# Kernel tuning notes

Hardware: AMD Instinct MI355X
Metric: run time of the kernel (lower is better)

## Reference

```python
import jax, jax.numpy as jnp
import numpy as np

N_NODES = 50000
N_EDGES = 1_600_000
N_DIMS = 64
INTERACT = ((0,), (1,), (0, 1))  # interact index tuples over [hidden_vi, hidden_vj]


def setup_inputs() -> dict:
    key = jax.random.key(0)
    k1, k2, k3 = jax.random.split(key, 3)
    hidden = jax.random.normal(k1, (1, N_NODES, N_DIMS), dtype=jnp.float32)
    pos_weight = jax.random.uniform(k2, (len(INTERACT), N_DIMS), dtype=jnp.float32)
    neg_weight = jax.random.uniform(k3, (len(INTERACT), N_DIMS), dtype=jnp.float32)
    rng = np.random.default_rng(0)
    vi = np.sort(rng.integers(0, N_NODES, size=N_EDGES)).astype(np.int32)  # sorted by vi
    vj = rng.integers(0, N_NODES, size=N_EDGES).astype(np.int32)
    rel = rng.integers(0, 500, size=N_EDGES).astype(np.int32)
    idx = np.zeros(N_EDGES, dtype=np.int32)  # batch_size == 1
    # (idx, vi, vj, rel, idx_vi, idx_vj, new_idx_e2vi, new_idx_e2vj)
    selected_edges = np.stack([idx, vi, vj, rel, vi, vj, vi, vj], axis=1)
    return {
        "hidden": hidden,
        "pos_weight": pos_weight,
        "neg_weight": neg_weight,
        "selected_edges": jnp.asarray(selected_edges),
    }


def _scorer(inputs, pos_weight, neg_weight):
    # inputs: list of [E, D]; returns per-edge scalar logits [E]
    pos_xs, neg_xs = [], []
    for idxs in INTERACT:
        pos_x = jnp.ones((), jnp.float32)
        neg_x = jnp.ones((), jnp.float32)
        for i in idxs:
            pos_x = pos_x * jnp.maximum(inputs[i], 0)
            neg_x = neg_x * (-jnp.minimum(inputs[i], 0))
        pos_xs.append(pos_x)
        neg_xs.append(neg_x)
    pos_xs = jnp.stack(pos_xs, axis=-2)  # [E, n_prod, D]
    neg_xs = jnp.stack(neg_xs, axis=-2)
    logits = jnp.sum(pos_xs * pos_weight, axis=(-2, -1)) - jnp.sum(neg_xs * neg_weight, axis=(-2, -1))
    return logits  # [E]


def reference(hidden, pos_weight, neg_weight, selected_edges):
    n_nodes = hidden.shape[1]
    vi = selected_edges[:, 1]
    vj = selected_edges[:, 2]
    h = hidden[0]  # [N, D], batch_size == 1

    # node2edge gather
    hidden_vi = h[vi]  # [E, D]
    hidden_vj = h[vj]  # [E, D]

    # per-edge attention logits (Scorer)
    logits = _scorer([hidden_vi, hidden_vj], pos_weight, neg_weight)  # [E]

    # neighbor softmax over outgoing edges of vi (sparse segment softmax)
    seg_max = jax.ops.segment_max(logits, vi, num_segments=n_nodes)
    ex = jnp.exp(logits - seg_max[vi])
    denom = jax.ops.segment_sum(ex, vi, num_segments=n_nodes)
    attn = ex / denom[vi]  # [E]

    # aggregate attended messages at vj and scatter back to node tensor
    msg = attn[:, None] * hidden_vi  # [E, D]
    out = jax.ops.segment_sum(msg, vj, num_segments=n_nodes)  # [N, D]
    return out[None]  # [1, N, D]
```

## Files before the change

kernel.cpp:

```cpp
#include <hip/hip_runtime.h>
#include <math.h>

#define NDIM 64

__device__ __forceinline__ unsigned bf16rne(unsigned u) {
    return (u + 0x7fffu + ((u >> 16) & 1u)) >> 16;
}

__global__ void __launch_bounds__(256)
k_prep_pack(const float* __restrict__ h,
            const float* __restrict__ pw, const float* __restrict__ nw,
            unsigned short* __restrict__ h16, float2* __restrict__ s12,
            const int* __restrict__ edges, unsigned* __restrict__ pvivj,
            int* __restrict__ hist,
            int n_nodes, int n_edges, int node_blocks) {
    if ((int)blockIdx.x < node_blocks) {
        const int lane = threadIdx.x & 63;
        const int n = blockIdx.x * 4 + (threadIdx.x >> 6);
        if (n >= n_nodes) return;
        const float a = h[(size_t)n * NDIM + lane];
        const float pa = fmaxf(a, 0.f), na = pa - a;
        float t1 = pa * pw[lane]      - na * nw[lane];
        float t2 = pa * pw[64 + lane] - na * nw[64 + lane];
        #pragma unroll
        for (int m = 32; m >= 1; m >>= 1) {
            t1 += __shfl_xor(t1, m, 64);
            t2 += __shfl_xor(t2, m, 64);
        }
        h16[(size_t)n * NDIM + lane] = (unsigned short)bf16rne(__float_as_uint(a));
        if (lane == 0) s12[n] = make_float2(t1, t2);
    } else {
        const int e = ((int)blockIdx.x - node_blocks) * 256 + threadIdx.x;
        if (e >= n_edges) return;
        const int vi = __builtin_nontemporal_load(edges + (size_t)e * 8 + 1);
        const int vj = __builtin_nontemporal_load(edges + (size_t)e * 8 + 2);
        __builtin_nontemporal_store((unsigned)vi | ((unsigned)vj << 16), pvivj + e);
        atomicAdd(&hist[vj], 1);
    }
}

__global__ void __launch_bounds__(256)
scan_blocks(int* __restrict__ data, int* __restrict__ bsum, int n) {
    __shared__ int sm[256];
    const int t = threadIdx.x;
    const int i = blockIdx.x * 256 + t;
    int v = (i < n) ? data[i] : 0;
    sm[t] = v;
    __syncthreads();
    int x = v;
    #pragma unroll
    for (int off = 1; off < 256; off <<= 1) {
        int add = (t >= off) ? sm[t - off] : 0;
        __syncthreads();
        x += add; sm[t] = x;
        __syncthreads();
    }
    if (i < n) data[i] = x - v;
    if (t == 255) bsum[blockIdx.x] = x;
}

__global__ void __launch_bounds__(256)
scan_top(int* __restrict__ bsum, int nb) {
    __shared__ int sm[256];
    const int t = threadIdx.x;
    const int chunk = (nb + 255) / 256;
    const int beg = t * chunk, end = min(beg + chunk, nb);
    int s = 0;
    for (int i = beg; i < end; ++i) s += bsum[i];
    sm[t] = s;
    __syncthreads();
    int x = s;
    #pragma unroll
    for (int off = 1; off < 256; off <<= 1) {
        int add = (t >= off) ? sm[t - off] : 0;
        __syncthreads();
        x += add; sm[t] = x;
        __syncthreads();
    }
    int run = x - s;
    for (int i = beg; i < end; ++i) { const int v = bsum[i]; bsum[i] = run; run += v; }
}

__global__ void __launch_bounds__(256)
scan_add(int* __restrict__ data, const int* __restrict__ bsum, int n, int total) {
    const int i = blockIdx.x * 256 + threadIdx.x;
    if (i < n) data[i] += bsum[blockIdx.x];
    else if (i == n) data[i] = total;
}

__global__ void __launch_bounds__(256)
k1_fused2(const unsigned* __restrict__ pvivj,
          const unsigned short* __restrict__ h16,
          const float2* __restrict__ s12,
          const float* __restrict__ w2p, const float* __restrict__ w2n,
          float* __restrict__ ex,
          int* __restrict__ offs,
          unsigned* __restrict__ rec,
          int n_edges) {
    const int t = blockIdx.x * 256 + threadIdx.x;
    const int e0 = t * 2;
    if (e0 >= n_edges) return;
    const bool has1 = (e0 + 1 < n_edges);

    const unsigned v0 = pvivj[e0];
    const unsigned v1 = has1 ? pvivj[e0 + 1] : v0;
    const int vi0 = (int)(v0 & 0xffffu), vj0 = (int)(v0 >> 16);
    const int vi1 = (int)(v1 & 0xffffu), vj1 = (int)(v1 >> 16);

    const uint4* hj0 = (const uint4*)(h16 + (size_t)vj0 * NDIM);
    const uint4* hj1 = (const uint4*)(h16 + (size_t)vj1 * NDIM);
    const uint4* hi0 = (const uint4*)(h16 + (size_t)vi0 * NDIM);
    const uint4* hi1 = (const uint4*)(h16 + (size_t)vi1 * NDIM);

    uint4 B0[8], B1[8];
    #pragma unroll
    for (int q = 0; q < 8; ++q) { B0[q] = hj0[q]; B1[q] = hj1[q]; }

    float cp0 = 0.f, cn0 = 0.f, cp1 = 0.f, cn1 = 0.f;
    #pragma unroll
    for (int q = 0; q < 8; ++q) {
        const uint4 ua0 = hi0[q];
        const uint4 ua1 = hi1[q];
        const unsigned a0u[4] = {ua0.x, ua0.y, ua0.z, ua0.w};
        const unsigned a1u[4] = {ua1.x, ua1.y, ua1.z, ua1.w};
        const unsigned b0u[4] = {B0[q].x, B0[q].y, B0[q].z, B0[q].w};
        const unsigned b1u[4] = {B1[q].x, B1[q].y, B1[q].z, B1[q].w};
        #pragma unroll
        for (int k = 0; k < 4; ++k) {
            const int d = q * 8 + k * 2;
            const float w2pd = w2p[d], w2pd1 = w2p[d + 1];
            const float w2nd = w2n[d], w2nd1 = w2n[d + 1];
            {
                const float a0 = __uint_as_float(a0u[k] << 16);
                const float a1 = __uint_as_float(a0u[k] & 0xffff0000u);
                const float b0 = __uint_as_float(b0u[k] << 16);
                const float b1 = __uint_as_float(b0u[k] & 0xffff0000u);
                const float pa0 = fmaxf(a0, 0.f), na0 = pa0 - a0;
                const float pb0 = fmaxf(b0, 0.f), nb0 = pb0 - b0;
                const float pa1 = fmaxf(a1, 0.f), na1 = pa1 - a1;
                const float pb1 = fmaxf(b1, 0.f), nb1 = pb1 - b1;
                cp0 = fmaf(pa0 * pb0, w2pd,  cp0);
                cn0 = fmaf(na0 * nb0, w2nd,  cn0);
                cp0 = fmaf(pa1 * pb1, w2pd1, cp0);
                cn0 = fmaf(na1 * nb1, w2nd1, cn0);
            }
            {
                const float a0 = __uint_as_float(a1u[k] << 16);
                const float a1 = __uint_as_float(a1u[k] & 0xffff0000u);
                const float b0 = __uint_as_float(b1u[k] << 16);
                const float b1 = __uint_as_float(b1u[k] & 0xffff0000u);
                const float pa0 = fmaxf(a0, 0.f), na0 = pa0 - a0;
                const float pb0 = fmaxf(b0, 0.f), nb0 = pb0 - b0;
                const float pa1 = fmaxf(a1, 0.f), na1 = pa1 - a1;
                const float pb1 = fmaxf(b1, 0.f), nb1 = pb1 - b1;
                cp1 = fmaf(pa0 * pb0, w2pd,  cp1);
                cn1 = fmaf(na0 * nb0, w2nd,  cn1);
                cp1 = fmaf(pa1 * pb1, w2pd1, cp1);
                cn1 = fmaf(na1 * nb1, w2nd1, cn1);
            }
        }
    }
    const float2 si0 = s12[vi0], sj0 = s12[vj0];
    const float2 si1 = s12[vi1], sj1 = s12[vj1];
    const float exf0 = __expf(si0.x + sj0.y + cp0 - cn0);
    const float exf1 = __expf(si1.x + sj1.y + cp1 - cn1);

    __builtin_nontemporal_store(exf0, ex + e0);
    const int pos0 = atomicAdd(&offs[vj0], 1);
    rec[pos0] = ((unsigned)vi0 << 16) | bf16rne(__float_as_uint(exf0));
    if (has1) {
        __builtin_nontemporal_store(exf1, ex + e0 + 1);
        const int pos1 = atomicAdd(&offs[vj1], 1);
        rec[pos1] = ((unsigned)vi1 << 16) | bf16rne(__float_as_uint(exf1));
    }
}

__global__ void __launch_bounds__(256)
k2_seg(const unsigned* __restrict__ pvivj, const float* __restrict__ ex,
       float* __restrict__ denom, int n_edges) {
    const int e = blockIdx.x * 256 + threadIdx.x;
    const int lane = threadIdx.x & 63;
    const bool valid = (e < n_edges);
    const int vi = valid ? (int)(pvivj[e] & 0xffffu) : -1;
    float s = valid ? ex[e] : 0.f;
    #pragma unroll
    for (int o = 1; o < 64; o <<= 1) {
        const float pv = __shfl_up(s, o, 64);
        const int   pi = __shfl_up(vi, o, 64);
        if (lane >= o && pi == vi) s += pv;
    }
    const int nvi = __shfl_down(vi, 1, 64);
    if ((lane == 63 || nvi != vi) && vi >= 0)
        atomicAdd(&denom[vi], s);
}

__global__ void __launch_bounds__(256)
k_gmul(const unsigned short* __restrict__ h16, const float* __restrict__ denom,
       unsigned short* __restrict__ g16, int n_nodes) {
    const int lane = threadIdx.x & 63;
    const int n = blockIdx.x * 4 + (threadIdx.x >> 6);
    if (n >= n_nodes) return;
    const float d = denom[n];
    const float r = (d > 0.f) ? 1.f / d : 0.f;
    const float hv = __uint_as_float((unsigned)h16[(size_t)n * NDIM + lane] << 16);
    g16[(size_t)n * NDIM + lane] = (unsigned short)bf16rne(__float_as_uint(hv * r));
}

__global__ void __launch_bounds__(256)
k3b_gather(const unsigned* __restrict__ rec, const int* __restrict__ offs,
           const unsigned short* __restrict__ g16,
           float* __restrict__ out, int n_nodes) {
    const int lane = threadIdx.x & 63;
    const int n = blockIdx.x * 4 + (threadIdx.x >> 6);
    if (n >= n_nodes) return;
    const int beg = (n == 0) ? 0 : offs[n - 1];
    const int end = offs[n];
    float acc = 0.f;
    int k = beg;
    for (; k + 8 <= end; k += 8) {
        unsigned r[8];
        #pragma unroll
        for (int u = 0; u < 8; ++u) r[u] = __builtin_nontemporal_load(rec + k + u);
        float v[8];
        #pragma unroll
        for (int u = 0; u < 8; ++u)
            v[u] = __uint_as_float((unsigned)g16[(size_t)(r[u] >> 16) * NDIM + lane] << 16);
        #pragma unroll
        for (int u = 0; u < 8; ++u)
            acc = fmaf(__uint_as_float(r[u] << 16), v[u], acc);
    }
    for (; k + 4 <= end; k += 4) {
        unsigned r[4];
        #pragma unroll
        for (int u = 0; u < 4; ++u) r[u] = __builtin_nontemporal_load(rec + k + u);
        #pragma unroll
        for (int u = 0; u < 4; ++u)
            acc = fmaf(__uint_as_float(r[u] << 16),
                       __uint_as_float((unsigned)g16[(size_t)(r[u] >> 16) * NDIM + lane] << 16), acc);
    }
    for (; k < end; ++k) {
        const unsigned r = __builtin_nontemporal_load(rec + k);
        acc = fmaf(__uint_as_float(r << 16),
                   __uint_as_float((unsigned)g16[(size_t)(r >> 16) * NDIM + lane] << 16), acc);
    }
    __builtin_nontemporal_store(acc, out + (size_t)n * NDIM + lane);
}

__device__ __forceinline__ float edge_term(float a, float b,
                                           float w0, float w1, float w2,
                                           float w3, float w4, float w5) {
    const float pa = fmaxf(a, 0.f), na = pa - a;
    const float pb = fmaxf(b, 0.f), nb = pb - b;
    return pa * w0 + pb * w1 + (pa * pb) * w2
         - (na * w3 + nb * w4 + (na * nb) * w5);
}

__global__ void __launch_bounds__(256)
k1_full_c(const int* __restrict__ edges, const float* __restrict__ h,
          const float* __restrict__ pw, const float* __restrict__ nw,
          float* __restrict__ ex, int* __restrict__ hist, int n_edges) {
    const int e = blockIdx.x * 256 + threadIdx.x;
    if (e >= n_edges) return;
    const int vi = edges[(size_t)e * 8 + 1];
    const int vj = edges[(size_t)e * 8 + 2];
    const float4* hi = (const float4*)(h + (size_t)vi * NDIM);
    const float4* hj = (const float4*)(h + (size_t)vj * NDIM);
    float c = 0.f;
    #pragma unroll 4
    for (int q = 0; q < 16; ++q) {
        const float4 a = hi[q];
        const float4 b = hj[q];
        const int d = q * 4;
        c += edge_term(a.x, b.x, pw[d],     pw[64 + d],     pw[128 + d],
                                 nw[d],     nw[64 + d],     nw[128 + d]);
        c += edge_term(a.y, b.y, pw[d + 1], pw[64 + d + 1], pw[128 + d + 1],
                                 nw[d + 1], nw[64 + d + 1], nw[128 + d + 1]);
        c += edge_term(a.z, b.z, pw[d + 2], pw[64 + d + 2], pw[128 + d + 2],
                                 nw[d + 2], nw[64 + d + 2], nw[128 + d + 2]);
        c += edge_term(a.w, b.w, pw[d + 3], pw[64 + d + 3], pw[128 + d + 3],
                                 nw[d + 3], nw[64 + d + 3], nw[128 + d + 3]);
    }
    ex[e] = __expf(c);
    atomicAdd(&hist[vj], 1);
}

__global__ void __launch_bounds__(256)
k2_denom_c(const int* __restrict__ edges, const float* __restrict__ ex,
           float* __restrict__ rdenom, int n_edges, int n_nodes) {
    const int n = blockIdx.x * 256 + threadIdx.x;
    if (n >= n_nodes) return;
    int lo = 0, hi = n_edges;
    while (lo < hi) { int mid = (lo + hi) >> 1; if (edges[(size_t)mid * 8 + 1] < n) lo = mid + 1; else hi = mid; }
    const int beg = lo;
    hi = n_edges;
    while (lo < hi) { int mid = (lo + hi) >> 1; if (edges[(size_t)mid * 8 + 1] < n + 1) lo = mid + 1; else hi = mid; }
    const int end = lo;
    float s = 0.f;
    for (int e = beg; e < end; ++e) s += ex[e];
    rdenom[n] = (end > beg) ? 1.f / s : 0.f;
}

__global__ void __launch_bounds__(256)
k3a_scatter_c(const int* __restrict__ edges, const float* __restrict__ ex,
              const float* __restrict__ rdenom,
              int* __restrict__ offs, int2* __restrict__ rec8, int n_edges) {
    const int e = blockIdx.x * 256 + threadIdx.x;
    if (e >= n_edges) return;
    const int vi = edges[(size_t)e * 8 + 1];
    const int vj = edges[(size_t)e * 8 + 2];
    const float attn = ex[e] * rdenom[vi];
    const int pos = atomicAdd(&offs[vj], 1);
    rec8[pos] = make_int2(vi, __float_as_int(attn));
}

__global__ void __launch_bounds__(256)
k3b_gather_c(const int2* __restrict__ rec8, const int* __restrict__ offs,
             const float* __restrict__ h, float* __restrict__ out, int n_nodes) {
    const int lane = threadIdx.x & 63;
    const int n = blockIdx.x * 4 + (threadIdx.x >> 6);
    if (n >= n_nodes) return;
    const int beg = (n == 0) ? 0 : offs[n - 1];
    const int end = offs[n];
    float acc = 0.f;
    for (int k = beg; k < end; ++k) {
        const int2 r = rec8[k];
        acc = fmaf(__int_as_float(r.y), h[(size_t)r.x * NDIM + lane], acc);
    }
    out[(size_t)n * NDIM + lane] = acc;
}

extern "C" void kernel_launch(void* const* d_in, const int* in_sizes, int n_in,
                              void* d_out, int out_size, void* d_ws, size_t ws_size,
                              hipStream_t stream) {
    const float* h   = (const float*)d_in[0];
    const float* pw  = (const float*)d_in[1];
    const float* nw  = (const float*)d_in[2];
    const int* edges = (const int*)d_in[3];
    float* out = (float*)d_out;

    const int n_nodes = in_sizes[0] / NDIM;
    const int n_edges = in_sizes[3] / 8;
    const size_t E = (size_t)n_edges, N = (size_t)n_nodes;

    const size_t szPv = E * 4, szRec = E * 4, szEx = E * 4;
    const size_t szH16 = N * NDIM * 2, szG16 = N * NDIM * 2, szS12 = N * 8;
    const size_t szOffs = (N + 1) * 4, szDen = N * 4, szB = 16384;
    const size_t need_A = szPv + szRec + szEx + szH16 + szG16 + szS12 + szOffs + szDen + szB;
    const bool tierA = (ws_size >= need_A) && (n_nodes <= 65536);

    const int eb  = (n_edges + 255) / 256;
    const int nbN = (n_nodes + 255) / 256;
    const int nw4 = (n_nodes + 3) / 4;

    if (tierA) {
        char* p = (char*)d_ws;
        unsigned* pvivj = (unsigned*)p;           p += szPv;
        unsigned* rec   = (unsigned*)p;           p += szRec;
        float*    ex    = (float*)p;              p += szEx;
        unsigned short* h16 = (unsigned short*)p; p += szH16;
        unsigned short* g16 = (unsigned short*)p; p += szG16;
        float2* s12   = (float2*)p;               p += szS12;
        int*    offs  = (int*)p;                  p += szOffs;
        float*  denom = (float*)p;                p += szDen;
        int*    bsum  = (int*)p;                  p += szB;

        hipMemsetAsync(offs, 0, szOffs + szDen, stream);

        k_prep_pack<<<nw4 + eb, 256, 0, stream>>>(h, pw, nw, h16, s12,
                                                  edges, pvivj, offs,
                                                  n_nodes, n_edges, nw4);
        scan_blocks<<<nbN, 256, 0, stream>>>(offs, bsum, n_nodes);
        scan_top<<<1, 256, 0, stream>>>(bsum, nbN);
        scan_add<<<(n_nodes + 1 + 255) / 256, 256, 0, stream>>>(offs, bsum, n_nodes, n_edges);

        const int npairs = (n_edges + 1) / 2;
        k1_fused2<<<(npairs + 255) / 256, 256, 0, stream>>>(pvivj, h16, s12,
                                                            pw + 128, nw + 128,
                                                            ex, offs, rec, n_edges);
        k2_seg<<<eb, 256, 0, stream>>>(pvivj, ex, denom, n_edges);
        k_gmul<<<nw4, 256, 0, stream>>>(h16, denom, g16, n_nodes);
        k3b_gather<<<nw4, 256, 0, stream>>>(rec, offs, g16, out, n_nodes);
    } else {
        char* p = (char*)d_ws;
        float* ex    = (float*)p;  p += E * 4;
        int2*  rec8  = (int2*)p;   p += E * 8;
        int*   offs  = (int*)p;    p += (N + 1) * 4;
        float* rdenom = (float*)p; p += N * 4;
        int*   bsum  = (int*)p;    p += 16384;

        hipMemsetAsync(offs, 0, (N + 1) * 4, stream);
        k1_full_c<<<eb, 256, 0, stream>>>(edges, h, pw, nw, ex, offs, n_edges);
        scan_blocks<<<nbN, 256, 0, stream>>>(offs, bsum, n_nodes);
        scan_top<<<1, 256, 0, stream>>>(bsum, nbN);
        scan_add<<<(n_nodes + 1 + 255) / 256, 256, 0, stream>>>(offs, bsum, n_nodes, n_edges);
        k2_denom_c<<<nbN, 256, 0, stream>>>(edges, ex, rdenom, n_edges, n_nodes);
        k3a_scatter_c<<<eb, 256, 0, stream>>>(edges, ex, rdenom, offs, rec8, n_edges);
        k3b_gather_c<<<nw4, 256, 0, stream>>>(rec8, offs, h, out, n_nodes);
    }
}
```

Baseline: 247.1 us.

## Fuse segment denominator reduction into edge scoring kernel, drop ex buffer

```diff
diff --git a/kernel.cpp b/kernel.cpp
--- a/kernel.cpp
+++ b/kernel.cpp
@@ -93,17 +93,20 @@
           const unsigned short* __restrict__ h16,
           const float2* __restrict__ s12,
           const float* __restrict__ w2p, const float* __restrict__ w2n,
-          float* __restrict__ ex,
+          float* __restrict__ denom,
           int* __restrict__ offs,
           unsigned* __restrict__ rec,
           int n_edges) {
     const int t = blockIdx.x * 256 + threadIdx.x;
+    const int lane = threadIdx.x & 63;
     const int e0 = t * 2;
-    if (e0 >= n_edges) return;
-    const bool has1 = (e0 + 1 < n_edges);
-
-    const unsigned v0 = pvivj[e0];
-    const unsigned v1 = has1 ? pvivj[e0 + 1] : v0;
+    const bool valid0 = (e0 < n_edges);
+    const bool valid1 = (e0 + 1 < n_edges);
+    const int ee0 = valid0 ? e0 : (n_edges - 1);
+    const int ee1 = valid1 ? (e0 + 1) : ee0;
+
+    const unsigned v0 = pvivj[ee0];
+    const unsigned v1 = pvivj[ee1];
     const int vi0 = (int)(v0 & 0xffffu), vj0 = (int)(v0 >> 16);
     const int vi1 = (int)(v1 & 0xffffu), vj1 = (int)(v1 >> 16);
 
@@ -162,36 +165,48 @@
     }
     const float2 si0 = s12[vi0], sj0 = s12[vj0];
     const float2 si1 = s12[vi1], sj1 = s12[vj1];
-    const float exf0 = __expf(si0.x + sj0.y + cp0 - cn0);
-    const float exf1 = __expf(si1.x + sj1.y + cp1 - cn1);
-
-    __builtin_nontemporal_store(exf0, ex + e0);
-    const int pos0 = atomicAdd(&offs[vj0], 1);
-    rec[pos0] = ((unsigned)vi0 << 16) | bf16rne(__float_as_uint(exf0));
-    if (has1) {
-        __builtin_nontemporal_store(exf1, ex + e0 + 1);
+    const float exf0 = valid0 ? __expf(si0.x + sj0.y + cp0 - cn0) : 0.f;
+    const float exf1 = valid1 ? __expf(si1.x + sj1.y + cp1 - cn1) : 0.f;
+
+    if (valid0) {
+        const int pos0 = atomicAdd(&offs[vj0], 1);
+        __builtin_nontemporal_store(((unsigned)vi0 << 16) | bf16rne(__float_as_uint(exf0)), rec + pos0);
+    }
+    if (valid1) {
         const int pos1 = atomicAdd(&offs[vj1], 1);
-        rec[pos1] = ((unsigned)vi1 << 16) | bf16rne(__float_as_uint(exf1));
-    }
-}
-
-__global__ void __launch_bounds__(256)
-k2_seg(const unsigned* __restrict__ pvivj, const float* __restrict__ ex,
-       float* __restrict__ denom, int n_edges) {
-    const int e = blockIdx.x * 256 + threadIdx.x;
-    const int lane = threadIdx.x & 63;
-    const bool valid = (e < n_edges);
-    const int vi = valid ? (int)(pvivj[e] & 0xffffu) : -1;
-    float s = valid ? ex[e] : 0.f;
+        __builtin_nontemporal_store(((unsigned)vi1 << 16) | bf16rne(__float_as_uint(exf1)), rec + pos1);
+    }
+
+    const int k0  = valid0 ? vi0 : -1;
+    const int k1v = valid1 ? vi1 : k0;
+    const float x0 = exf0, x1 = exf1;
+    const float tl = (k0 == k1v) ? (x0 + x1) : x1;
+
+    int prev_k1 = __shfl_up(k1v, 1, 64);
+    if (lane == 0) prev_k1 = -2;
+
+    float s = tl;
+    bool  f = !(k0 == k1v && k0 == prev_k1);
     #pragma unroll
     for (int o = 1; o < 64; o <<= 1) {
-        const float pv = __shfl_up(s, o, 64);
-        const int   pi = __shfl_up(vi, o, 64);
-        if (lane >= o && pi == vi) s += pv;
-    }
-    const int nvi = __shfl_down(vi, 1, 64);
-    if ((lane == 63 || nvi != vi) && vi >= 0)
-        atomicAdd(&denom[vi], s);
+        const float ps = __shfl_up(s, o, 64);
+        const int   pf = __shfl_up((int)f, o, 64);
+        if (lane >= o) {
+            if (!f) s += ps;
+            f = f || (pf != 0);
+        }
+    }
+    const float s_prev = __shfl_up(s, 1, 64);
+
+    if (k0 >= 0 && k0 != k1v) {
+        float sum0 = x0;
+        if (lane > 0 && prev_k1 == k0) sum0 += s_prev;
+        atomicAdd(&denom[k0], sum0);
+    }
+    int next_k0 = __shfl_down(k0, 1, 64);
+    const bool tail_end = (lane == 63) || (next_k0 != k1v);
+    if (k1v >= 0 && tail_end)
+        atomicAdd(&denom[k1v], s);
 }
 
 __global__ void __launch_bounds__(256)
@@ -217,16 +232,16 @@
     const int end = offs[n];
     float acc = 0.f;
     int k = beg;
-    for (; k + 8 <= end; k += 8) {
-        unsigned r[8];
-        #pragma unroll
-        for (int u = 0; u < 8; ++u) r[u] = __builtin_nontemporal_load(rec + k + u);
-        float v[8];
-        #pragma unroll
-        for (int u = 0; u < 8; ++u)
+    for (; k + 16 <= end; k += 16) {
+        unsigned r[16];
+        #pragma unroll
+        for (int u = 0; u < 16; ++u) r[u] = __builtin_nontemporal_load(rec + k + u);
+        float v[16];
+        #pragma unroll
+        for (int u = 0; u < 16; ++u)
             v[u] = __uint_as_float((unsigned)g16[(size_t)(r[u] >> 16) * NDIM + lane] << 16);
         #pragma unroll
-        for (int u = 0; u < 8; ++u)
+        for (int u = 0; u < 16; ++u)
             acc = fmaf(__uint_as_float(r[u] << 16), v[u], acc);
     }
     for (; k + 4 <= end; k += 4) {
@@ -342,10 +357,10 @@
     const int n_edges = in_sizes[3] / 8;
     const size_t E = (size_t)n_edges, N = (size_t)n_nodes;
 
-    const size_t szPv = E * 4, szRec = E * 4, szEx = E * 4;
+    const size_t szPv = E * 4, szRec = E * 4;
     const size_t szH16 = N * NDIM * 2, szG16 = N * NDIM * 2, szS12 = N * 8;
     const size_t szOffs = (N + 1) * 4, szDen = N * 4, szB = 16384;
-    const size_t need_A = szPv + szRec + szEx + szH16 + szG16 + szS12 + szOffs + szDen + szB;
+    const size_t need_A = szPv + szRec + szH16 + szG16 + szS12 + szOffs + szDen + szB;
     const bool tierA = (ws_size >= need_A) && (n_nodes <= 65536);
 
     const int eb  = (n_edges + 255) / 256;
@@ -356,7 +371,6 @@
         char* p = (char*)d_ws;
         unsigned* pvivj = (unsigned*)p;           p += szPv;
         unsigned* rec   = (unsigned*)p;           p += szRec;
-        float*    ex    = (float*)p;              p += szEx;
         unsigned short* h16 = (unsigned short*)p; p += szH16;
         unsigned short* g16 = (unsigned short*)p; p += szG16;
         float2* s12   = (float2*)p;               p += szS12;
@@ -376,8 +390,7 @@
         const int npairs = (n_edges + 1) / 2;
         k1_fused2<<<(npairs + 255) / 256, 256, 0, stream>>>(pvivj, h16, s12,
                                                             pw + 128, nw + 128,
-                                                            ex, offs, rec, n_edges);
-        k2_seg<<<eb, 256, 0, stream>>>(pvivj, ex, denom, n_edges);
+                                                            denom, offs, rec, n_edges);
         k_gmul<<<nw4, 256, 0, stream>>>(h16, denom, g16, n_nodes);
         k3b_gather<<<nw4, 256, 0, stream>>>(rec, offs, g16, out, n_nodes);
     } else {
```

New measurement: 262.9 us. 1.06x slower.
